# Optimization experiments

Hardware: AMD Instinct MI355X
Metric: run time of the kernel (lower is better)

Reference implementation:

```python
import jax, jax.numpy as jnp
import numpy as np

NUM_USERS = 100000
NUM_ITEMS = 50000
N_NODES = NUM_USERS + NUM_ITEMS
EMB_DIM = 64
N_LAYERS = 3
NNZ = 4800000


def setup_inputs() -> dict:
    key = jax.random.key(0)
    k1, k2, k3, k4, k5 = jax.random.split(key, 5)
    user_emb = jax.random.normal(k1, (NUM_USERS, EMB_DIM), dtype=jnp.float32)
    item_emb = jax.random.normal(k2, (NUM_ITEMS, EMB_DIM), dtype=jnp.float32)
    adj_rows = jax.random.randint(k3, (NNZ,), 0, N_NODES, dtype=jnp.int32)
    adj_cols = jax.random.randint(k4, (NNZ,), 0, N_NODES, dtype=jnp.int32)
    adj_vals = jax.random.uniform(k5, (NNZ,), dtype=jnp.float32)
    return {"user_emb": user_emb, "item_emb": item_emb,
            "adj_rows": adj_rows, "adj_cols": adj_cols, "adj_vals": adj_vals}


def _spmm(rows, cols, vals, x):
    # COO SpMM: out[r] += vals * x[c]   (gather + weighted segment-sum)
    return jax.ops.segment_sum(vals[:, None] * x[cols], rows,
                               num_segments=N_NODES)


def reference(user_emb, item_emb, adj_rows, adj_cols, adj_vals):
    all_emb = jnp.concatenate([user_emb, item_emb], axis=0)  # [N, D]
    acc = all_emb
    cur = all_emb
    for _ in range(N_LAYERS):
        cur = _spmm(adj_rows, adj_cols, adj_vals, cur)
        acc = acc + cur
    out = acc / jnp.float32(N_LAYERS + 1)  # mean over stacked layer outputs
    users = out[:NUM_USERS]
    items = out[NUM_USERS:]
    return users, items
```

## Files before the change

kernel.cpp:

```cpp
#include <hip/hip_runtime.h>
#include <hip/hip_fp16.h>

#define NUM_USERS 100000
#define NUM_ITEMS 50000
#define N_NODES   150000
#define EMB_DIM   64
#define NNZ       4800000
#define N_LAYERS  3

#define TILE_ROWS 256
#define TILE_SHIFT 8
#define NTILES    ((N_NODES + TILE_ROWS - 1) / TILE_ROWS)
#define COL_BITS  18
#define COL_MASK  ((1 << COL_BITS) - 1)
#define VAL_BITS  14
#define VAL_MASK  ((1 << VAL_BITS) - 1)
#define PAD       10240

static constexpr size_t TOTAL = (size_t)N_NODES * EMB_DIM;

typedef long long ll1;

__global__ void lgcn_init_h(const float4* __restrict__ user_emb,
                            const float4* __restrict__ item_emb,
                            uint2* __restrict__ cur16) {
    size_t i = (size_t)blockIdx.x * blockDim.x + threadIdx.x;
    const size_t n4 = TOTAL / 4;
    if (i >= n4) return;
    const size_t ub4 = (size_t)NUM_USERS * EMB_DIM / 4;
    float4 v = (i < ub4) ? user_emb[i] : item_emb[i - ub4];
    __half2 h0 = __floats2half2_rn(v.x, v.y);
    __half2 h1 = __floats2half2_rn(v.z, v.w);
    uint2 u;
    u.x = *reinterpret_cast<unsigned int*>(&h0);
    u.y = *reinterpret_cast<unsigned int*>(&h1);
    cur16[i] = u;
}

#define BKT_BLK 1024
#define EPB     8192

__global__ __launch_bounds__(BKT_BLK) void
edge_bucket(const int* __restrict__ rows, const int* __restrict__ cols,
            const float* __restrict__ vals, int* __restrict__ tile_cursor,
            int2* __restrict__ ebuf1) {
    __shared__ int2 stage[EPB];
    __shared__ int  dstIdx[EPB];
    __shared__ int  hcur[NTILES];
    __shared__ int  lbase[NTILES];
    __shared__ int  gbase[NTILES];

    int tid = threadIdx.x;
    size_t blockStart = (size_t)blockIdx.x * EPB;

    int r[8]; int c[8]; float v[8];
    for (int i = tid; i < NTILES; i += BKT_BLK) hcur[i] = 0;
    __syncthreads();

    #pragma unroll
    for (int k = 0; k < 8; k++) {
        size_t e = blockStart + (size_t)k * BKT_BLK + tid;
        if (e < NNZ) {
            r[k] = __builtin_nontemporal_load(&rows[e]);
            c[k] = __builtin_nontemporal_load(&cols[e]);
            v[k] = __builtin_nontemporal_load(&vals[e]);
            atomicAdd(&hcur[r[k] >> TILE_SHIFT], 1);
        } else r[k] = -1;
    }
    __syncthreads();

    int cnt = (tid < NTILES) ? hcur[tid] : 0;
    for (int off = 1; off < 1024; off <<= 1) {
        int add = (tid >= off && tid < NTILES) ? hcur[tid - off] : 0;
        __syncthreads();
        if (tid < NTILES) hcur[tid] += add;
        __syncthreads();
    }
    if (tid < NTILES) {
        int ex = hcur[tid] - cnt;
        lbase[tid] = ex;
        gbase[tid] = cnt ? (tid * PAD + atomicAdd(&tile_cursor[tid], cnt)) : 0;
    }
    __syncthreads();
    if (tid < NTILES) hcur[tid] = lbase[tid];
    __syncthreads();

    #pragma unroll
    for (int k = 0; k < 8; k++) {
        if (r[k] >= 0) {
            int t = r[k] >> TILE_SHIFT;
            int slot = atomicAdd(&hcur[t], 1);
            stage[slot] = make_int2(((r[k] & (TILE_ROWS - 1)) << COL_BITS) | c[k],
                                    __float_as_int(v[k]));
            dstIdx[slot] = gbase[t] + (slot - lbase[t]);
        }
    }
    __syncthreads();

    int total = (int)min((size_t)EPB, (size_t)NNZ - blockStart);
    for (int i = tid; i < total; i += BKT_BLK)
        ebuf1[dstIdx[i]] = stage[i];
}

__global__ void tile_scan(const int* __restrict__ counts,
                          int* __restrict__ tile_ptr,
                          int* __restrict__ row_ptr) {
    __shared__ int s[1024];
    int t = threadIdx.x;
    int v = (t < NTILES) ? counts[t] : 0;
    s[t] = v;
    __syncthreads();
    for (int off = 1; off < 1024; off <<= 1) {
        int add = (t >= off) ? s[t - off] : 0;
        __syncthreads();
        s[t] += add;
        __syncthreads();
    }
    if (t < NTILES) tile_ptr[t] = s[t] - v;
    if (t == 0) {
        tile_ptr[NTILES] = NNZ;
        row_ptr[N_NODES] = NNZ;
    }
}

#define RS_BLK 512

__global__ __launch_bounds__(RS_BLK) void
row_sort(const int2* __restrict__ ebuf1, const int* __restrict__ tile_ptr,
         int* __restrict__ row_ptr, unsigned int* __restrict__ epack) {
    __shared__ int hist[TILE_ROWS];
    __shared__ int cur256[TILE_ROWS];
    int tid = threadIdx.x;
    int tile = blockIdx.x;
    int base_in = tile * PAD;
    int obase = tile_ptr[tile];
    int cnt = tile_ptr[tile + 1] - obase;
    const ll1* eb64 = reinterpret_cast<const ll1*>(ebuf1);

    if (tid < TILE_ROWS) hist[tid] = 0;
    __syncthreads();

    for (int i = tid; i < cnt; i += RS_BLK) {
        ll1 raw = __builtin_nontemporal_load(&eb64[base_in + i]);
        unsigned int mx = (unsigned int)(unsigned long long)raw;
        atomicAdd(&hist[mx >> COL_BITS], 1);
    }
    __syncthreads();

    int v = (tid < TILE_ROWS) ? hist[tid] : 0;
    for (int off = 1; off < TILE_ROWS; off <<= 1) {
        int add = (tid >= off && tid < TILE_ROWS) ? hist[tid - off] : 0;
        __syncthreads();
        if (tid < TILE_ROWS) hist[tid] += add;
        __syncthreads();
    }
    if (tid < TILE_ROWS) {
        int excl = hist[tid] - v;
        int rowG = tile * TILE_ROWS + tid;
        if (rowG < N_NODES) row_ptr[rowG] = obase + excl;
        cur256[tid] = obase + excl;
    }
    __syncthreads();

    for (int i = tid; i < cnt; i += RS_BLK) {
        ll1 raw = __builtin_nontemporal_load(&eb64[base_in + i]);
        unsigned int mx = (unsigned int)(unsigned long long)raw;
        unsigned int my = (unsigned int)((unsigned long long)raw >> 32);
        int r = mx >> COL_BITS;
        int pos = atomicAdd(&cur256[r], 1);
        unsigned int col = mx & COL_MASK;
        unsigned int hb = (unsigned)__half_as_ushort(__float2half_rn(__uint_as_float(my)));
        if (hb > (unsigned)VAL_MASK) hb = VAL_MASK;
        epack[pos] = (col << VAL_BITS) | hb;
    }
}

__device__ __forceinline__ void edge_fma(unsigned int m, const uint4* __restrict__ x16v,
                                         int t, __half2& a0, __half2& a1,
                                         __half2& a2, __half2& a3) {
    uint4 xv = x16v[(size_t)(m >> VAL_BITS) * 8 + t];
    unsigned int vv = (m & VAL_MASK);
    vv |= (vv << 16);
    __half2 vh = *reinterpret_cast<__half2*>(&vv);
    const __half2* xh = reinterpret_cast<const __half2*>(&xv);
    a0 = __hfma2(xh[0], vh, a0);
    a1 = __hfma2(xh[1], vh, a1);
    a2 = __hfma2(xh[2], vh, a2);
    a3 = __hfma2(xh[3], vh, a3);
}

template <int FINAL>
__global__ void lgcn_spmm_h8(const int* __restrict__ row_ptr,
                             const unsigned int* __restrict__ edges,
                             const uint4* __restrict__ x16v,
                             uint4* __restrict__ y16v,
                             const uint4* __restrict__ x0v,
                             const uint4* __restrict__ y1v,
                             const uint4* __restrict__ y2v,
                             float4* __restrict__ outv) {
    int wid = blockIdx.x * (blockDim.x >> 6) + (threadIdx.x >> 6);
    if (wid >= N_NODES) return;
    int lane = threadIdx.x & 63;
    int g = lane >> 3;
    int t = lane & 7;
    int e  = row_ptr[wid];
    int e1 = row_ptr[wid + 1];

    __half2 a0 = __float2half2_rn(0.0f), a1 = a0, a2 = a0, a3 = a0;

    for (; e + 16 <= e1; e += 16) {
        unsigned int mA = edges[e + g];
        unsigned int mB = edges[e + 8 + g];
        uint4 xvA = x16v[(size_t)(mA >> VAL_BITS) * 8 + t];
        uint4 xvB = x16v[(size_t)(mB >> VAL_BITS) * 8 + t];
        unsigned int vA = (mA & VAL_MASK); vA |= (vA << 16);
        unsigned int vB = (mB & VAL_MASK); vB |= (vB << 16);
        __half2 vhA = *reinterpret_cast<__half2*>(&vA);
        __half2 vhB = *reinterpret_cast<__half2*>(&vB);
        const __half2* xhA = reinterpret_cast<const __half2*>(&xvA);
        const __half2* xhB = reinterpret_cast<const __half2*>(&xvB);
        a0 = __hfma2(xhA[0], vhA, a0);
        a1 = __hfma2(xhA[1], vhA, a1);
        a2 = __hfma2(xhA[2], vhA, a2);
        a3 = __hfma2(xhA[3], vhA, a3);
        a0 = __hfma2(xhB[0], vhB, a0);
        a1 = __hfma2(xhB[1], vhB, a1);
        a2 = __hfma2(xhB[2], vhB, a2);
        a3 = __hfma2(xhB[3], vhB, a3);
    }
    if (e + 8 <= e1) {
        edge_fma(edges[e + g], x16v, t, a0, a1, a2, a3);
        e += 8;
    }
    int rem = e1 - e;
    if (g < rem) {
        edge_fma(edges[e + g], x16v, t, a0, a1, a2, a3);
    }

    #pragma unroll
    for (int mask = 8; mask <= 32; mask <<= 1) {
        unsigned int u;
        u = __shfl_xor(*reinterpret_cast<unsigned int*>(&a0), mask);
        a0 = __hadd2(a0, *reinterpret_cast<__half2*>(&u));
        u = __shfl_xor(*reinterpret_cast<unsigned int*>(&a1), mask);
        a1 = __hadd2(a1, *reinterpret_cast<__half2*>(&u));
        u = __shfl_xor(*reinterpret_cast<unsigned int*>(&a2), mask);
        a2 = __hadd2(a2, *reinterpret_cast<__half2*>(&u));
        u = __shfl_xor(*reinterpret_cast<unsigned int*>(&a3), mask);
        a3 = __hadd2(a3, *reinterpret_cast<__half2*>(&u));
    }

    if (lane < 8) {
        size_t idx = (size_t)wid * 8 + t;
        if (!FINAL) {
            uint4 u;
            u.x = *reinterpret_cast<unsigned int*>(&a0);
            u.y = *reinterpret_cast<unsigned int*>(&a1);
            u.z = *reinterpret_cast<unsigned int*>(&a2);
            u.w = *reinterpret_cast<unsigned int*>(&a3);
            y16v[idx] = u;
        } else {
            uint4 ux = x0v[idx];
            uint4 u1 = y1v[idx];
            uint4 u2 = y2v[idx];
            const __half2* hx = reinterpret_cast<const __half2*>(&ux);
            const __half2* h1 = reinterpret_cast<const __half2*>(&u1);
            const __half2* h2 = reinterpret_cast<const __half2*>(&u2);
            __half2 av[4] = {a0, a1, a2, a3};
            float o[8];
            #pragma unroll
            for (int k = 0; k < 4; k++) {
                float2 fx = __half22float2(hx[k]);
                float2 f1 = __half22float2(h1[k]);
                float2 f2 = __half22float2(h2[k]);
                float2 fa = __half22float2(av[k]);
                o[2*k]   = (fx.x + f1.x + f2.x + fa.x) * 0.25f;
                o[2*k+1] = (fx.y + f1.y + f2.y + fa.y) * 0.25f;
            }
            float4 o0 = make_float4(o[0], o[1], o[2], o[3]);
            float4 o1 = make_float4(o[4], o[5], o[6], o[7]);
            outv[(size_t)wid * 16 + 2*t]     = o0;
            outv[(size_t)wid * 16 + 2*t + 1] = o1;
        }
    }
}

__global__ void lgcn_init_f(const float4* __restrict__ user_emb,
                            const float4* __restrict__ item_emb,
                            float4* __restrict__ cur,
                            float4* __restrict__ acc) {
    size_t i = (size_t)blockIdx.x * blockDim.x + threadIdx.x;
    const size_t n4 = TOTAL / 4;
    if (i >= n4) return;
    const size_t ub4 = (size_t)NUM_USERS * EMB_DIM / 4;
    float4 v = (i < ub4) ? user_emb[i] : item_emb[i - ub4];
    cur[i] = v;
    acc[i] = v;
}

__global__ void lgcn_spmm_scatter(const int* __restrict__ rows,
                                  const int* __restrict__ cols,
                                  const float* __restrict__ vals,
                                  const float* __restrict__ x,
                                  float* __restrict__ y) {
    size_t t = (size_t)blockIdx.x * blockDim.x + threadIdx.x;
    if (t >= (size_t)NNZ * EMB_DIM) return;
    int e = (int)(t >> 6);
    int d = (int)(t & 63);
    atomicAdd(&y[(size_t)rows[e] * EMB_DIM + d], vals[e] * x[(size_t)cols[e] * EMB_DIM + d]);
}

__global__ void lgcn_accum(float4* __restrict__ acc, const float4* __restrict__ nxt, float scale) {
    size_t i = (size_t)blockIdx.x * blockDim.x + threadIdx.x;
    const size_t n4 = TOTAL / 4;
    if (i >= n4) return;
    float4 a = acc[i]; float4 b = nxt[i];
    a.x = (a.x + b.x) * scale; a.y = (a.y + b.y) * scale;
    a.z = (a.z + b.z) * scale; a.w = (a.w + b.w) * scale;
    acc[i] = a;
}

extern "C" void kernel_launch(void* const* d_in, const int* in_sizes, int n_in,
                              void* d_out, int out_size, void* d_ws, size_t ws_size,
                              hipStream_t stream) {
    const float* user_emb = (const float*)d_in[0];
    const float* item_emb = (const float*)d_in[1];
    const int*   rows     = (const int*)d_in[2];
    const int*   cols     = (const int*)d_in[3];
    const float* vals     = (const float*)d_in[4];
    float* out = (float*)d_out;

    const int BLK = 256;
    const size_t n4 = TOTAL / 4;
    dim3 g_init((n4 + BLK - 1) / BLK);

    char* p = (char*)d_ws;
    unsigned int* epack = (unsigned int*)p;  p += (size_t)NNZ * sizeof(unsigned int);
    __half* y1 = (__half*)p;
    int2*   ebuf1 = (int2*)p;                p += (size_t)NTILES * PAD * sizeof(int2);
    __half* y2 = y1 + TOTAL;
    __half* cur16 = (__half*)p;              p += TOTAL * sizeof(__half);
    int*    tile_ptr = (int*)p;              p += (size_t)(NTILES + 1) * sizeof(int);
    int*    tile_cursor = (int*)p;           p += (size_t)NTILES * sizeof(int);
    int*    row_ptr = (int*)p;               p += (size_t)(N_NODES + 1) * sizeof(int);
    size_t needed = (size_t)(p - (char*)d_ws);

    if (ws_size < needed) {
        float* fcur = (float*)d_ws;
        float* fnxt = fcur + TOTAL;
        lgcn_init_f<<<g_init, BLK, 0, stream>>>((const float4*)user_emb, (const float4*)item_emb,
                                                (float4*)fcur, (float4*)out);
        const size_t st = (size_t)NNZ * EMB_DIM;
        dim3 g_scat((st + BLK - 1) / BLK);
        for (int l = 0; l < N_LAYERS; ++l) {
            hipMemsetAsync(fnxt, 0, TOTAL * sizeof(float), stream);
            lgcn_spmm_scatter<<<g_scat, BLK, 0, stream>>>(rows, cols, vals, fcur, fnxt);
            float scale = (l == N_LAYERS - 1) ? (1.0f / (N_LAYERS + 1)) : 1.0f;
            lgcn_accum<<<g_init, BLK, 0, stream>>>((float4*)out, (const float4*)fnxt, scale);
            float* t = fcur; fcur = fnxt; fnxt = t;
        }
        return;
    }

    hipMemsetAsync(tile_cursor, 0, (size_t)NTILES * sizeof(int), stream);
    int nBuckBlocks = (NNZ + EPB - 1) / EPB;
    edge_bucket<<<nBuckBlocks, BKT_BLK, 0, stream>>>(rows, cols, vals, tile_cursor, ebuf1);
    tile_scan<<<1, 1024, 0, stream>>>(tile_cursor, tile_ptr, row_ptr);
    row_sort<<<NTILES, RS_BLK, 0, stream>>>(ebuf1, tile_ptr, row_ptr, epack);

    lgcn_init_h<<<g_init, BLK, 0, stream>>>((const float4*)user_emb, (const float4*)item_emb,
                                            (uint2*)cur16);

    const int WAVES_PER_BLK = BLK / 64;
    dim3 g_spmm((N_NODES + WAVES_PER_BLK - 1) / WAVES_PER_BLK);
    lgcn_spmm_h8<0><<<g_spmm, BLK, 0, stream>>>(row_ptr, epack,
        (const uint4*)cur16, (uint4*)y1, nullptr, nullptr, nullptr, nullptr);
    lgcn_spmm_h8<0><<<g_spmm, BLK, 0, stream>>>(row_ptr, epack,
        (const uint4*)y1, (uint4*)y2, nullptr, nullptr, nullptr, nullptr);
    lgcn_spmm_h8<1><<<g_spmm, BLK, 0, stream>>>(row_ptr, epack,
        (const uint4*)y2, nullptr,
        (const uint4*)cur16, (const uint4*)y1, (const uint4*)y2, (float4*)out);
}
```

Measured before the change: 379.5 us.

## Bucket edges by column range within each row during row sort

Extends the per-tile counting sort so edges are binned by row and by a coarse column bucket (32 buckets of 8192 columns) rather than by row alone. The scan becomes a two-level per-thread-plus-block prefix over 8192 bins. The intent is to order each row's edges by column region so the SpMM gathers of embedding rows hit nearby memory and reuse L2/MALL better. In exchange, shared memory use grows to about 34KB per block, which may lower occupancy of the sort kernel. The scan also adds extra work.

```diff
diff --git a/kernel.cpp b/kernel.cpp
--- a/kernel.cpp
+++ b/kernel.cpp
@@ -16,6 +16,10 @@
 #define VAL_BITS  14
 #define VAL_MASK  ((1 << VAL_BITS) - 1)
 #define PAD       10240
+
+#define CB_SHIFT  13
+#define NBKT      32
+#define NBINS     (TILE_ROWS * NBKT)
 
 static constexpr size_t TOTAL = (size_t)N_NODES * EMB_DIM;
 
@@ -124,12 +128,13 @@
 }
 
 #define RS_BLK 512
+#define BINS_PER_THREAD (NBINS / RS_BLK)
 
 __global__ __launch_bounds__(RS_BLK) void
 row_sort(const int2* __restrict__ ebuf1, const int* __restrict__ tile_ptr,
          int* __restrict__ row_ptr, unsigned int* __restrict__ epack) {
-    __shared__ int hist[TILE_ROWS];
-    __shared__ int cur256[TILE_ROWS];
+    __shared__ int hist[NBINS];
+    __shared__ int tsum[RS_BLK];
     int tid = threadIdx.x;
     int tile = blockIdx.x;
     int base_in = tile * PAD;
@@ -137,28 +142,41 @@
     int cnt = tile_ptr[tile + 1] - obase;
     const ll1* eb64 = reinterpret_cast<const ll1*>(ebuf1);
 
-    if (tid < TILE_ROWS) hist[tid] = 0;
+    for (int i = tid; i < NBINS; i += RS_BLK) hist[i] = 0;
     __syncthreads();
 
     for (int i = tid; i < cnt; i += RS_BLK) {
         ll1 raw = __builtin_nontemporal_load(&eb64[base_in + i]);
         unsigned int mx = (unsigned int)(unsigned long long)raw;
-        atomicAdd(&hist[mx >> COL_BITS], 1);
-    }
-    __syncthreads();
-
-    int v = (tid < TILE_ROWS) ? hist[tid] : 0;
-    for (int off = 1; off < TILE_ROWS; off <<= 1) {
-        int add = (tid >= off && tid < TILE_ROWS) ? hist[tid - off] : 0;
-        __syncthreads();
-        if (tid < TILE_ROWS) hist[tid] += add;
-        __syncthreads();
-    }
-    if (tid < TILE_ROWS) {
-        int excl = hist[tid] - v;
-        int rowG = tile * TILE_ROWS + tid;
-        if (rowG < N_NODES) row_ptr[rowG] = obase + excl;
-        cur256[tid] = obase + excl;
+        int r = mx >> COL_BITS;
+        int b = (mx & COL_MASK) >> CB_SHIFT;
+        atomicAdd(&hist[(r << 5) | b], 1);
+    }
+    __syncthreads();
+
+    int base = tid * BINS_PER_THREAD;
+    int local[BINS_PER_THREAD];
+    int s = 0;
+    #pragma unroll
+    for (int k = 0; k < BINS_PER_THREAD; k++) { local[k] = s; s += hist[base + k]; }
+    tsum[tid] = s;
+    __syncthreads();
+    for (int off = 1; off < RS_BLK; off <<= 1) {
+        int add = (tid >= off) ? tsum[tid - off] : 0;
+        __syncthreads();
+        tsum[tid] += add;
+        __syncthreads();
+    }
+    int toff = tsum[tid] - s;
+    #pragma unroll
+    for (int k = 0; k < BINS_PER_THREAD; k++)
+        hist[base + k] = obase + toff + local[k];
+    __syncthreads();
+
+    if ((base & (NBKT - 1)) == 0) {
+        int r = base >> 5;
+        int rowG = tile * TILE_ROWS + r;
+        if (rowG < N_NODES) row_ptr[rowG] = hist[base];
     }
     __syncthreads();
 
@@ -167,7 +185,8 @@
         unsigned int mx = (unsigned int)(unsigned long long)raw;
         unsigned int my = (unsigned int)((unsigned long long)raw >> 32);
         int r = mx >> COL_BITS;
-        int pos = atomicAdd(&cur256[r], 1);
+        int b = (mx & COL_MASK) >> CB_SHIFT;
+        int pos = atomicAdd(&hist[(r << 5) | b], 1);
         unsigned int col = mx & COL_MASK;
         unsigned int hb = (unsigned)__half_as_ushort(__float2half_rn(__uint_as_float(my)));
         if (hb > (unsigned)VAL_MASK) hb = VAL_MASK;
```

New measurement: 381.6 us. About the same (+0.6%).
